# Kernel tuning notes

Measured on AMD Instinct MI355X. Metric: run time of the kernel, lower is better.

Reference implementation:

```python
import jax, jax.numpy as jnp
import numpy as np
import math

B, S, E, D = 8, 2048, 1024, 1024  # batch, seq, emb_dim, encoder_emb_dim
LN_EPS = 1e-5
CLAMP = 1.0e9

def setup_inputs() -> dict:
    key = jax.random.key(0)
    ks = jax.random.split(key, 6)
    s = 1.0 / math.sqrt(E)
    return {
        "x": jax.random.normal(ks[0], (B, S, E), dtype=jnp.float32),
        "ln_w": jnp.ones((E,), jnp.float32),
        "ln_b": jnp.zeros((E,), jnp.float32),
        "wq": jax.random.normal(ks[1], (E, D), jnp.float32) * s,
        "bq": jnp.zeros((D,), jnp.float32),
        "wk": jax.random.normal(ks[2], (E, D), jnp.float32) * s,
        "bk": jnp.zeros((D,), jnp.float32),
        "wv": jax.random.normal(ks[3], (E, D), jnp.float32) * s,
        "bv": jnp.zeros((D,), jnp.float32),
        "w0": jax.random.normal(ks[4], (D, E), jnp.float32) * (1.0 / math.sqrt(D)),
        "b0": jnp.zeros((E,), jnp.float32),
    }

def reference(x, ln_w, ln_b, wq, bq, wk, bk, wv, bv, w0, b0):
    # LayerNorm over last dim (torch default eps=1e-5)
    mu = jnp.mean(x, axis=-1, keepdims=True)
    var = jnp.mean(jnp.square(x - mu), axis=-1, keepdims=True)
    xn = (x - mu) * jax.lax.rsqrt(var + LN_EPS) * ln_w + ln_b

    q = xn @ wq + bq  # [B,S,D]
    k = xn @ wk + bk
    v = xn @ wv + bv

    scale = math.sqrt(D) + 1e-9
    scores = jnp.einsum("bsd,btd->bst", q, k) / scale
    scores = jnp.clip(scores, -CLAMP, CLAMP)

    # masking=True, self_attending=True: mask = tril(ones, diagonal=-1)
    # i.e. positions t < s get -inf; diagonal stays unmasked (no NaN rows).
    mask = jnp.tril(jnp.ones((S, S), dtype=bool), k=-1)
    scores = jnp.where(mask, -jnp.inf, scores)

    a = jax.nn.softmax(scores, axis=-1)
    h = jnp.einsum("bst,btd->bsd", a, v)
    return h @ w0 + b0
```

## Files before the change

### kernel.cpp

```cpp
#include <hip/hip_runtime.h>
#include <cmath>

using u16 = unsigned short;
using u32 = unsigned int;
using bf16x8 = __attribute__((ext_vector_type(8))) __bf16;
using f32x4  = __attribute__((ext_vector_type(4))) float;

__device__ inline u16 f2bf(float f) {
  u32 u = __float_as_uint(f);
  u32 r = (u + 0x7fffu + ((u >> 16) & 1u)) >> 16;
  return (u16)r;
}
__device__ inline float bf2f(u16 v) { return __uint_as_float(((u32)v) << 16); }

__global__ __launch_bounds__(256) void prep1(
    const float* __restrict__ x, const float* __restrict__ lnw,
    const float* __restrict__ lnb, const float* __restrict__ wq,
    const float* __restrict__ wk, const float* __restrict__ wv,
    const float* __restrict__ w0, const float* __restrict__ bq,
    const float* __restrict__ bk, const float* __restrict__ bv,
    u16* __restrict__ xn, u16* __restrict__ w0t, u16* __restrict__ wqb,
    u16* __restrict__ wkb, u16* __restrict__ wvb, float* __restrict__ uvec,
    float* __restrict__ vvec, float* __restrict__ wb, float* __restrict__ sb) {
  int b = blockIdx.x;
  int tid = threadIdx.x;
  __shared__ float red[4];
  __shared__ float red2[4];
  int lane = tid & 63, wave = tid >> 6;
  if (b < 16384) {
    const float4* xr = (const float4*)(x + (size_t)b * 1024);
    float4 v = xr[tid];
    float s  = v.x + v.y + v.z + v.w;
    float ss = v.x * v.x + v.y * v.y + v.z * v.z + v.w * v.w;
#pragma unroll
    for (int o = 32; o >= 1; o >>= 1) {
      s  += __shfl_xor(s, o, 64);
      ss += __shfl_xor(ss, o, 64);
    }
    if (lane == 0) { red[wave] = s; red2[wave] = ss; }
    __syncthreads();
    s  = red[0] + red[1] + red[2] + red[3];
    ss = red2[0] + red2[1] + red2[2] + red2[3];
    float mean = s * (1.0f / 1024.0f);
    float var  = ss * (1.0f / 1024.0f) - mean * mean;
    float rstd = rsqrtf(var + 1e-5f);
    int c = tid * 4;
    ushort4 ov;
    ov.x = f2bf((v.x - mean) * rstd * lnw[c + 0] + lnb[c + 0]);
    ov.y = f2bf((v.y - mean) * rstd * lnw[c + 1] + lnb[c + 1]);
    ov.z = f2bf((v.z - mean) * rstd * lnw[c + 2] + lnb[c + 2]);
    ov.w = f2bf((v.w - mean) * rstd * lnw[c + 3] + lnb[c + 3]);
    ((ushort4*)(xn + (size_t)b * 1024))[tid] = ov;
  } else if (b < 17408) {
    int b2 = b - 16384;
    int c0 = (b2 & 31) * 32, r0 = (b2 >> 5) * 32;
    int tx = tid & 31, ty = tid >> 5;
    __shared__ float tile[32][33];
#pragma unroll
    for (int i = 0; i < 32; i += 8)
      tile[ty + i][tx] = w0[(size_t)(r0 + ty + i) * 1024 + c0 + tx];
    __syncthreads();
#pragma unroll
    for (int i = 0; i < 32; i += 8)
      w0t[(size_t)(c0 + ty + i) * 1024 + r0 + tx] = f2bf(tile[tx][ty + i]);
  } else if (b < 18944) {
    int b3 = b - 17408;
    int mat = b3 / 512, blk = b3 % 512;
    const float* src = (mat == 0) ? wq : (mat == 1) ? wk : wv;
    u16* dst = (mat == 0) ? wqb : (mat == 1) ? wkb : wvb;
    size_t base = (size_t)blk * 2048 + (size_t)tid * 8;
#pragma unroll
    for (int i = 0; i < 8; ++i) dst[base + i] = f2bf(src[base + i]);
  } else if (b < 22016) {
    int b4 = b - 18944;
    int which = b4 >> 10, idx = b4 & 1023;
    float p = 0.f;
    if (which == 0) {
      const float* r = wq + (size_t)idx * 1024;
      for (int e = tid * 4; e < (tid + 1) * 4; ++e) p += r[e] * bk[e];
    } else if (which == 1) {
      const float* r = wk + (size_t)idx * 1024;
      for (int e = tid * 4; e < (tid + 1) * 4; ++e) p += r[e] * bq[e];
    } else {
      for (int d = tid * 4; d < (tid + 1) * 4; ++d)
        p += bv[d] * w0[(size_t)d * 1024 + idx];
    }
#pragma unroll
    for (int o = 32; o >= 1; o >>= 1) p += __shfl_xor(p, o, 64);
    if (lane == 0) red[wave] = p;
    __syncthreads();
    if (tid == 0) {
      float t = red[0] + red[1] + red[2] + red[3];
      if (which == 0) uvec[idx] = t;
      else if (which == 1) vvec[idx] = t;
      else wb[idx] = t;
    }
  } else {
    float p = 0.f;
    for (int e = tid * 4; e < (tid + 1) * 4; ++e) p += bq[e] * bk[e];
#pragma unroll
    for (int o = 32; o >= 1; o >>= 1) p += __shfl_xor(p, o, 64);
    if (lane == 0) red[wave] = p;
    __syncthreads();
    if (tid == 0) sb[0] = red[0] + red[1] + red[2] + red[3];
  }
}

__global__ __launch_bounds__(512) void ruv_kernel(
    const u16* __restrict__ xn, const float* __restrict__ uvec,
    const float* __restrict__ vvec, const float* __restrict__ sb,
    float* __restrict__ ru, float* __restrict__ rv) {
  int wv = threadIdx.x >> 6, lane = threadIdx.x & 63;
  int r = blockIdx.x * 8 + wv;
  const u16* row = xn + (size_t)r * 1024;
  int c0 = lane * 16;
  float pu = 0.f, pv = 0.f;
#pragma unroll
  for (int i = 0; i < 16; ++i) {
    float xv = bf2f(row[c0 + i]);
    pu += xv * uvec[c0 + i];
    pv += xv * vvec[c0 + i];
  }
#pragma unroll
  for (int o = 32; o >= 1; o >>= 1) {
    pu += __shfl_xor(pu, o, 64);
    pv += __shfl_xor(pv, o, 64);
  }
  if (lane == 0) { ru[r] = pu + sb[0]; rv[r] = pv; }
}

template <int OUTF32, int MODE>
__global__ __launch_bounds__(512, 2) void gemm256(
    const u16* __restrict__ A, const u16* __restrict__ B, void* __restrict__ Cv,
    const float* __restrict__ bias, int K, int lda, int ldb, int ldc,
    float scale, long long sA, long long sB, long long sC) {
  int gx = gridDim.x;
  int wg = blockIdx.y * gx + blockIdx.x;
  {
    int nwg = gx * gridDim.y;
    if ((nwg & 7) == 0) {
      int q = nwg >> 3;
      wg = (wg & 7) * q + (wg >> 3);
    }
  }
  const int ti = wg / gx, tj = wg % gx, bz = blockIdx.z;
  if (MODE == 1 && tj < ti) return;

  const u16* Ab = A + (size_t)bz * (size_t)sA;
  const u16* Bb = B + (size_t)bz * (size_t)sB;

  __shared__ u16 As[2][256 * 64];
  __shared__ u16 Bs[2][256 * 64];

  const int tid = threadIdx.x;
  const int wave = tid >> 6, lane = tid & 63;
  const int wr = wave >> 2, wc = wave & 3;
  const int fr = lane & 15;
  const int kb16 = (lane >> 4) * 16;
  const int swz = (fr & 7) << 4;
  const int cs0 = kb16 ^ swz;
  const int cs1 = (64 + kb16) ^ swz;
  const int aRowOff = (wr * 128 + fr) * 128;
  const int bRowOff = (wc * 64 + fr) * 128;

  size_t gAo[2][2], gBo[2][2];
  u32 ldsA[2][2], ldsB[2][2];
#pragma unroll
  for (int h = 0; h < 2; ++h) {
#pragma unroll
    for (int l = 0; l < 2; ++l) {
      int i = l * 512 + tid;
      int rih = i >> 3, ch8 = i & 7;
      int rA = (rih & 63) + ((rih >> 6) << 7) + h * 64;
      int cbA = (ch8 << 4) ^ ((rA & 7) << 4);
      gAo[h][l] = (size_t)rA * lda + (cbA >> 1);
      ldsA[h][l] = (u32)(rA * 8 + ch8) * 16;
      int rB = (rih & 31) + ((rih >> 5) << 6) + h * 32;
      int cbB = (ch8 << 4) ^ ((rB & 7) << 4);
      gBo[h][l] = (size_t)rB * ldb + (cbB >> 1);
      ldsB[h][l] = (u32)(rB * 8 + ch8) * 16;
    }
  }
  const size_t aBase = (size_t)(ti * 256) * lda;
  const size_t bBase = (size_t)(tj * 256) * ldb;

  const int k0 = (MODE == 2) ? ti * 256 : 0;
  const int niter = (K - k0) / 128;

  f32x4 acc[8][4] = {};
  bf16x8 aF[4][2], bF[4][2];

#define GLL(gaddr, laddr)                                        \
  __builtin_amdgcn_global_load_lds(                              \
      (const __attribute__((address_space(1))) void*)(gaddr),    \
      (__attribute__((address_space(3))) void*)(laddr), 16, 0, 0)

#define STAGE_A(buf, h, t)                                                     \
  do {                                                                         \
    const size_t _kt = aBase + (size_t)(k0 + (t) * 64);                        \
    GLL(Ab + _kt + gAo[h][0], (char*)&As[buf][0] + ldsA[h][0]);                \
    GLL(Ab + _kt + gAo[h][1], (char*)&As[buf][0] + ldsA[h][1]);                \
  } while (0)
#define STAGE_B(buf, h, t)                                                     \
  do {                                                                         \
    const size_t _kt = bBase + (size_t)(k0 + (t) * 64);                        \
    GLL(Bb + _kt + gBo[h][0], (char*)&Bs[buf][0] + ldsB[h][0]);                \
    GLL(Bb + _kt + gBo[h][1], (char*)&Bs[buf][0] + ldsB[h][1]);                \
  } while (0)

#define DS_A(buf, qm)                                                \
  do {                                                               \
    const char* _pa = (const char*)&As[buf][0] + aRowOff + (qm)*8192;\
    _Pragma("unroll") for (int mm = 0; mm < 4; ++mm) {               \
      aF[mm][0] = *(const bf16x8*)(_pa + mm * 2048 + cs0);           \
      aF[mm][1] = *(const bf16x8*)(_pa + mm * 2048 + cs1);           \
    }                                                                \
  } while (0)
#define DS_B(buf, nh)                                                \
  do {                                                               \
    const char* _pb = (const char*)&Bs[buf][0] + bRowOff;            \
    _Pragma("unroll") for (int nn = 0; nn < 2; ++nn) {               \
      bF[(nh)*2 + nn][0] = *(const bf16x8*)(_pb + ((nh)*2 + nn) * 2048 + cs0); \
      bF[(nh)*2 + nn][1] = *(const bf16x8*)(_pb + ((nh)*2 + nn) * 2048 + cs1); \
    }                                                                \
  } while (0)

#define MMA(qm, nh)                                                          \
  do {                                                                       \
    _Pragma("unroll") for (int mm = 0; mm < 4; ++mm)                         \
    _Pragma("unroll") for (int nn = 0; nn < 2; ++nn) {                       \
      f32x4 _c = acc[(qm)*4 + mm][(nh)*2 + nn];                              \
      _c = __builtin_amdgcn_mfma_f32_16x16x32_bf16(aF[mm][0], bF[(nh)*2+nn][0], _c, 0, 0, 0); \
      _c = __builtin_amdgcn_mfma_f32_16x16x32_bf16(aF[mm][1], bF[(nh)*2+nn][1], _c, 0, 0, 0); \
      acc[(qm)*4 + mm][(nh)*2 + nn] = _c;                                    \
    }                                                                        \
  } while (0)

#define BAR __builtin_amdgcn_s_barrier()
#define LGKM0 asm volatile("s_waitcnt lgkmcnt(0)" ::: "memory")
#define VM6 asm volatile("s_waitcnt vmcnt(6)" ::: "memory")
#define VM0 asm volatile("s_waitcnt vmcnt(0)" ::: "memory")
#define PRIO1 __builtin_amdgcn_s_setprio(1)
#define PRIO0 __builtin_amdgcn_s_setprio(0)

  STAGE_B(0, 0, 0); STAGE_B(0, 1, 0); STAGE_A(0, 0, 0); STAGE_A(0, 1, 0);
  STAGE_B(1, 0, 1); STAGE_B(1, 1, 1); STAGE_A(1, 0, 1);
  VM6; BAR;

  for (int it = 0; it < niter; ++it) {
    const bool last = (it == niter - 1);
    const int t1g = 2 * it + 1, t2g = 2 * it + 2, t3g = 2 * it + 3;

    DS_A(0, 0); DS_B(0, 0);
    STAGE_A(1, 1, t1g);
    BAR; LGKM0; PRIO1; MMA(0, 0); PRIO0; BAR;
    DS_B(0, 1);
    if (!last) STAGE_B(0, 0, t2g);
    BAR; LGKM0; PRIO1; MMA(0, 1); PRIO0; BAR;
    DS_A(0, 1);
    if (!last) STAGE_B(0, 1, t2g);
    BAR; LGKM0; PRIO1; MMA(1, 0); PRIO0; BAR;
    if (!last) STAGE_A(0, 0, t2g);
    BAR; PRIO1; MMA(1, 1); PRIO0;
    if (last) { VM0; } else { VM6; }
    BAR;
    DS_A(1, 0); DS_B(1, 0);
    if (!last) STAGE_A(0, 1, t2g);
    BAR; LGKM0; PRIO1; MMA(0, 0); PRIO0; BAR;
    DS_B(1, 1);
    if (!last) STAGE_B(1, 0, t3g);
    BAR; LGKM0; PRIO1; MMA(0, 1); PRIO0; BAR;
    DS_A(1, 1);
    if (!last) STAGE_B(1, 1, t3g);
    BAR; LGKM0; PRIO1; MMA(1, 0); PRIO0; BAR;
    if (!last) STAGE_A(1, 0, t3g);
    BAR; PRIO1; MMA(1, 1); PRIO0;
    if (!last) VM6;
    BAR;
  }

  const int orow0 = ti * 256 + wr * 128 + ((lane >> 4) << 2);
  const int ocol0 = tj * 256 + wc * 64 + fr;
#pragma unroll
  for (int m = 0; m < 8; ++m) {
#pragma unroll
    for (int n = 0; n < 4; ++n) {
      const int col = ocol0 + n * 16;
      const float bv = bias ? bias[col] : 0.0f;
#pragma unroll
      for (int j = 0; j < 4; ++j) {
        const int row = orow0 + m * 16 + j;
        const float v = acc[m][n][j] * scale + bv;
        const size_t idx = (size_t)bz * (size_t)sC + (size_t)row * ldc + col;
        if (OUTF32) ((float*)Cv)[idx] = v;
        else        ((u16*)Cv)[idx]   = f2bf(v);
      }
    }
  }
#undef GLL
#undef STAGE_A
#undef STAGE_B
#undef DS_A
#undef DS_B
#undef MMA
#undef BAR
#undef LGKM0
#undef VM6
#undef VM0
#undef PRIO1
#undef PRIO0
}

template <int BM, int EPI, int LDA, int LDB, int LDC, int KK, int K0CT>
__device__ __forceinline__ void gemm_body(
    const u16* __restrict__ Ab, const u16* __restrict__ Bb,
    void* __restrict__ Cp, const float* __restrict__ bias,
    const float* __restrict__ rbias, int rk0, float scale, size_t cbase,
    int ti, int tj, u16* __restrict__ AsP, u16* __restrict__ BsP,
    float* __restrict__ sumP, int dco,
    const float* __restrict__ ruP, const float* __restrict__ rvP) {
  constexpr int WM = BM / 2;
  constexpr int MH = BM / 64;
  constexpr int FM = 2 * MH;
  constexpr int HR = BM / 4;
  constexpr int LA = BM / 128;

  const int k0 = (K0CT >= 0) ? K0CT : rk0;

  const int tid = threadIdx.x;
  const int wave = tid >> 6, lane = tid & 63;
  const int wr = wave >> 2, wc = wave & 3;
  const int fr = lane & 15;
  const int kb16 = (lane >> 4) * 16;
  const int swz = (fr & 7) << 4;
  const int cs0 = kb16 ^ swz;
  const int cs1 = (64 + kb16) ^ swz;
  const int aRowOff = (wr * WM + fr) * 128;
  const int bRowOff = (wc * 64 + fr) * 128;

  __shared__ float invLds[(EPI == 2) ? BM : 1];
  if constexpr (EPI == 2) {
    if (tid < BM) {
      int s = ti * BM + tid;
      float a = 0.f;
      for (int q2 = s >> 8; q2 < 8; ++q2) a += sumP[q2 * 2048 + s];
      invLds[tid] = 1.0f / a;
    }
  }

  size_t gAo[2][LA], gBo[2][2];
  u32 ldsA[2][LA], ldsB[2][2];
#pragma unroll
  for (int h = 0; h < 2; ++h) {
#pragma unroll
    for (int l = 0; l < LA; ++l) {
      int i = l * 512 + tid;
      int rih = i >> 3, ch8 = i & 7;
      int rA = (rih % HR) + (rih / HR) * WM + h * HR;
      int cbA = (ch8 << 4) ^ ((rA & 7) << 4);
      gAo[h][l] = (size_t)rA * LDA + (cbA >> 1);
      ldsA[h][l] = (u32)(rA * 8 + ch8) * 16;
    }
#pragma unroll
    for (int l = 0; l < 2; ++l) {
      int i = l * 512 + tid;
      int rih = i >> 3, ch8 = i & 7;
      int rB = (rih & 31) + ((rih >> 5) << 6) + h * 32;
      int cbB = (ch8 << 4) ^ ((rB & 7) << 4);
      gBo[h][l] = (size_t)rB * LDB + (cbB >> 1);
      ldsB[h][l] = (u32)(rB * 8 + ch8) * 16;
    }
  }
  const size_t aBase = (size_t)(ti * BM) * LDA;
  const size_t bBase = (size_t)(tj * 256) * LDB;
  const int niter = (KK - k0) / 128;

  f32x4 acc[FM][4] = {};
  bf16x8 aF[MH][2], bF[4][2];

#define GLL(gaddr, laddr)                                        \
  __builtin_amdgcn_global_load_lds(                              \
      (const __attribute__((address_space(1))) void*)(gaddr),    \
      (__attribute__((address_space(3))) void*)(laddr), 16, 0, 0)

#define STAGE_A(buf, h, t)                                                   \
  do {                                                                       \
    const size_t _kt = aBase + (size_t)(k0 + (t) * 64);                      \
    _Pragma("unroll") for (int _l = 0; _l < LA; ++_l)                        \
        GLL(Ab + _kt + gAo[h][_l],                                           \
            (char*)(AsP + (buf) * (BM * 64)) + ldsA[h][_l]);                 \
  } while (0)
#define STAGE_B(buf, h, t)                                                   \
  do {                                                                       \
    const size_t _kt = bBase + (size_t)(k0 + (t) * 64);                      \
    _Pragma("unroll") for (int _l = 0; _l < 2; ++_l)                         \
        GLL(Bb + _kt + gBo[h][_l],                                           \
            (char*)(BsP + (buf) * (256 * 64)) + ldsB[h][_l]);                \
  } while (0)

#define DS_A(buf, qm)                                                        \
  do {                                                                       \
    const char* _pa =                                                        \
        (const char*)(AsP + (buf) * (BM * 64)) + aRowOff + (qm) * (MH * 2048); \
    _Pragma("unroll") for (int mm = 0; mm < MH; ++mm) {                      \
      aF[mm][0] = *(const bf16x8*)(_pa + mm * 2048 + cs0);                   \
      aF[mm][1] = *(const bf16x8*)(_pa + mm * 2048 + cs1);                   \
    }                                                                        \
  } while (0)
#define DS_B(buf, nh)                                                        \
  do {                                                                       \
    const char* _pb = (const char*)(BsP + (buf) * (256 * 64)) + bRowOff;     \
    _Pragma("unroll") for (int nn = 0; nn < 2; ++nn) {                       \
      bF[(nh)*2 + nn][0] = *(const bf16x8*)(_pb + ((nh)*2 + nn) * 2048 + cs0); \
      bF[(nh)*2 + nn][1] = *(const bf16x8*)(_pb + ((nh)*2 + nn) * 2048 + cs1); \
    }                                                                        \
  } while (0)

#define MMA(qm, nh)                                                          \
  do {                                                                       \
    _Pragma("unroll") for (int mm = 0; mm < MH; ++mm)                        \
    _Pragma("unroll") for (int nn = 0; nn < 2; ++nn) {                       \
      f32x4 _c = acc[(qm)*MH + mm][(nh)*2 + nn];                             \
      _c = __builtin_amdgcn_mfma_f32_16x16x32_bf16(aF[mm][0], bF[(nh)*2+nn][0], _c, 0, 0, 0); \
      _c = __builtin_amdgcn_mfma_f32_16x16x32_bf16(aF[mm][1], bF[(nh)*2+nn][1], _c, 0, 0, 0); \
      acc[(qm)*MH + mm][(nh)*2 + nn] = _c;                                   \
    }                                                                        \
  } while (0)

#define BAR __builtin_amdgcn_s_barrier()
#define LGKM0 asm volatile("s_waitcnt lgkmcnt(0)" ::: "memory")
#define VMN                                                                  \
  do {                                                                       \
    if constexpr (BM == 256)                                                 \
      asm volatile("s_waitcnt vmcnt(6)" ::: "memory");                       \
    else                                                                     \
      asm volatile("s_waitcnt vmcnt(5)" ::: "memory");                       \
  } while (0)
#define VM0 asm volatile("s_waitcnt vmcnt(0)" ::: "memory")
#define PRIO1 __builtin_amdgcn_s_setprio(1)
#define PRIO0 __builtin_amdgcn_s_setprio(0)

  STAGE_B(0, 0, 0); STAGE_B(0, 1, 0); STAGE_A(0, 0, 0); STAGE_A(0, 1, 0);
  STAGE_B(1, 0, 1); STAGE_B(1, 1, 1); STAGE_A(1, 0, 1);
  VMN; BAR;

#pragma unroll 1
  for (int it = 0; it < niter; ++it) {
    const bool last = (it == niter - 1);
    const int t1g = 2 * it + 1, t2g = 2 * it + 2, t3g = 2 * it + 3;

    DS_A(0, 0); DS_B(0, 0);
    STAGE_A(1, 1, t1g);
    BAR; LGKM0; PRIO1; MMA(0, 0); PRIO0; BAR;
    DS_B(0, 1);
    if (!last) STAGE_B(0, 0, t2g);
    BAR; LGKM0; PRIO1; MMA(0, 1); PRIO0; BAR;
    DS_A(0, 1);
    if (!last) STAGE_B(0, 1, t2g);
    BAR; LGKM0; PRIO1; MMA(1, 0); PRIO0; BAR;
    if (!last) STAGE_A(0, 0, t2g);
    BAR; PRIO1; MMA(1, 1); PRIO0;
    if (last) { VM0; } else { VMN; }
    BAR;
    DS_A(1, 0); DS_B(1, 0);
    if (!last) STAGE_A(0, 1, t2g);
    BAR; LGKM0; PRIO1; MMA(0, 0); PRIO0; BAR;
    DS_B(1, 1);
    if (!last) STAGE_B(1, 0, t3g);
    BAR; LGKM0; PRIO1; MMA(0, 1); PRIO0; BAR;
    DS_A(1, 1);
    if (!last) STAGE_B(1, 1, t3g);
    BAR; LGKM0; PRIO1; MMA(1, 0); PRIO0; BAR;
    if (!last) STAGE_A(1, 0, t3g);
    BAR; PRIO1; MMA(1, 1); PRIO0;
    if (!last) VMN;
    BAR;
  }

  const int orowL = wr * WM + ((lane >> 4) << 2);
  const int orow0 = ti * BM + orowL;
  const int ocol0 = tj * 256 + wc * 64 + fr;

  if constexpr (EPI == 1) {
    float* slds = (float*)AsP;
#pragma unroll
    for (int m = 0; m < FM; ++m) {
#pragma unroll
      for (int j = 0; j < 4; ++j) {
        const int rl = orowL + m * 16 + j;
        const int row = ti * BM + rl;
        const float ru = ruP[row];
        float rsum = 0.f;
#pragma unroll
        for (int n = 0; n < 4; ++n) {
          const int cl = wc * 64 + fr + n * 16;
          const int col = tj * 256 + cl;
          float v = (acc[m][n][j] + ru + rvP[col]) * scale;
          v = fminf(fmaxf(v, -1.0e9f), 1.0e9f);
          v = fminf(v, 60.0f);
          float e = __expf(v - 5.0f);
          if (cl < rl + dco) e = 0.f;
          rsum += e;
          ((u16*)Cp)[cbase + (size_t)row * LDC + col] = f2bf(e);
        }
        rsum += __shfl_xor(rsum, 1, 64);
        rsum += __shfl_xor(rsum, 2, 64);
        rsum += __shfl_xor(rsum, 4, 64);
        rsum += __shfl_xor(rsum, 8, 64);
        if (fr == 0) slds[rl * 4 + wc] = rsum;
      }
    }
    __syncthreads();
    if (tid < BM) {
      float t = slds[tid * 4 + 0] + slds[tid * 4 + 1] +
                slds[tid * 4 + 2] + slds[tid * 4 + 3];
      sumP[ti * BM + tid] = t;
    }
  } else {
#pragma unroll
    for (int m = 0; m < FM; ++m) {
#pragma unroll
      for (int j = 0; j < 4; ++j) {
        const int row = orow0 + m * 16 + j;
        float mul = (EPI == 2) ? invLds[orowL + m * 16 + j] : 1.0f;
        float rb = (EPI == 0 && rbias) ? rbias[row] : 0.0f;
#pragma unroll
        for (int n = 0; n < 4; ++n) {
          const int col = ocol0 + n * 16;
          const float bv = bias ? bias[col] : 0.0f;
          const size_t idx = cbase + (size_t)row * LDC + col;
          if constexpr (EPI == 2) {
            ((float*)Cp)[idx] = acc[m][n][j] * mul + bv;
          } else {
            ((u16*)Cp)[idx] = f2bf(acc[m][n][j] + bv + rb);
          }
        }
      }
    }
  }
#undef GLL
#undef STAGE_A
#undef STAGE_B
#undef DS_A
#undef DS_B
#undef MMA
#undef BAR
#undef LGKM0
#undef VMN
#undef VM0
#undef PRIO1
#undef PRIO0
}

__global__ __launch_bounds__(512, 2) void prep2(
    const u16* __restrict__ wqb, const u16* __restrict__ wkb,
    const u16* __restrict__ wvb, const u16* __restrict__ w0t,
    u16* __restrict__ Gt, u16* __restrict__ Uw) {
  __shared__ u16 As[2][128 * 64];
  __shared__ u16 Bs[2][256 * 64];
  int b = blockIdx.x;
  if (b < 32) {
    int ti = b & 7, tj = b >> 3;
    gemm_body<128, 0, 1024, 1024, 1024, 1024, 0>(
        wkb, wqb, Gt, nullptr, nullptr, 0, 1.0f, 0, ti, tj,
        &As[0][0], &Bs[0][0], nullptr, 0, nullptr, nullptr);
  } else {
    int b2 = b - 32;
    int ti = b2 & 7, tj = b2 >> 3;
    gemm_body<128, 0, 1024, 1024, 1024, 1024, 0>(
        w0t, wvb, Uw, nullptr, nullptr, 0, 1.0f, 0, ti, tj,
        &As[0][0], &Bs[0][0], nullptr, 0, nullptr, nullptr);
  }
}

__global__ __launch_bounds__(512, 2) void gemm_qkwt(
    const u16* __restrict__ xnG, const u16* __restrict__ xn,
    const u16* __restrict__ Uw, u16* __restrict__ Wt, u16* __restrict__ sc,
    float* __restrict__ sumP, const float* __restrict__ ru,
    const float* __restrict__ rv, const float* __restrict__ wb,
    int qkBlocks, int b0, int nb, float qk_scale) {
  __shared__ u16 As[2][256 * 64];
  __shared__ u16 Bs[2][256 * 64];
  const long long sXN = 2048LL * 1024, sWt = 1024LL * 2048, sS = 2048LL * 2048;
  int x = blockIdx.x;
  if (x < qkBlocks) {
    int bzl = x % nb, t36 = x / nb;
    int bz = b0 + bzl;
    int tq = 0, rem = t36;
    for (;;) { int L = 8 - tq; if (rem < L) break; rem -= L; ++tq; }
    int tj = tq + rem;
    gemm_body<256, 1, 1024, 1024, 2048, 1024, 0>(
        xnG + (size_t)bz * sXN, xn + (size_t)bz * sXN, sc, nullptr, nullptr,
        0, qk_scale, (size_t)bzl * sS, tq, tj, &As[0][0], &Bs[0][0],
        sumP + ((size_t)bz * 8 + tj) * 2048, (tq - tj) * 256,
        ru + (size_t)bz * 2048, rv + (size_t)bz * 2048);
  } else {
    int x2 = x - qkBlocks;
    int bz = x2 & 7;
    int o = x2 >> 3;
    int ti = o & 7, tj = o >> 3;
    gemm_body<128, 0, 1024, 1024, 2048, 1024, 0>(
        Uw, xn + (size_t)bz * sXN, Wt, nullptr, wb, 0, 1.0f,
        (size_t)bz * sWt, ti, tj, &As[0][0], &Bs[0][0],
        nullptr, 0, nullptr, nullptr);
  }
}

__global__ __launch_bounds__(512, 2) void gemm_pv(
    const u16* __restrict__ sc, const u16* __restrict__ Wt,
    float* __restrict__ out, const float* __restrict__ b0v,
    float* __restrict__ sumP, int nb, int bA) {
  __shared__ u16 As[2][128 * 64];
  __shared__ u16 Bs[2][256 * 64];
  int x = blockIdx.x;
  int bzl = x % nb;
  int rem = x / nb;
  int ti = rem >> 2, tj = rem & 3;
  int bz = bA + bzl;
  gemm_body<128, 2, 2048, 2048, 1024, 2048, -1>(
      sc + (size_t)bzl * 2048 * 2048, Wt + (size_t)bz * 1024 * 2048, out, b0v,
      nullptr, ti * 128, 1.0f, (size_t)bz * 2048 * 1024, ti, tj,
      &As[0][0], &Bs[0][0], sumP + (size_t)bz * 8 * 2048, 0,
      nullptr, nullptr);
}

extern "C" void kernel_launch(void* const* d_in, const int* in_sizes, int n_in,
                              void* d_out, int out_size, void* d_ws, size_t ws_size,
                              hipStream_t stream) {
  (void)in_sizes; (void)n_in; (void)out_size;
  const float* x   = (const float*)d_in[0];
  const float* lnw = (const float*)d_in[1];
  const float* lnb = (const float*)d_in[2];
  const float* wq  = (const float*)d_in[3];
  const float* bq  = (const float*)d_in[4];
  const float* wk  = (const float*)d_in[5];
  const float* bk  = (const float*)d_in[6];
  const float* wv  = (const float*)d_in[7];
  const float* bv  = (const float*)d_in[8];
  const float* w0  = (const float*)d_in[9];
  const float* b0  = (const float*)d_in[10];
  float* out = (float*)d_out;

  const size_t ROWS = 16384;
  char* ws = (char*)d_ws;
  size_t off = 0;
  auto alloc = [&](size_t bytes) -> void* {
    void* p = ws + off;
    off += (bytes + 255) & ~(size_t)255;
    return p;
  };
  u16*   xn   = (u16*)alloc(ROWS * 1024 * 2);
  u16*   w0t  = (u16*)alloc((size_t)1024 * 1024 * 2);
  u16*   wqb  = (u16*)alloc((size_t)1024 * 1024 * 2);
  u16*   wkb  = (u16*)alloc((size_t)1024 * 1024 * 2);
  u16*   wvb  = (u16*)alloc((size_t)1024 * 1024 * 2);
  u16*   Gt   = (u16*)alloc((size_t)1024 * 1024 * 2);
  u16*   Uw   = (u16*)alloc((size_t)1024 * 1024 * 2);
  float* uvec = (float*)alloc(1024 * 4);
  float* vvec = (float*)alloc(1024 * 4);
  float* wb   = (float*)alloc(1024 * 4);
  float* sb   = (float*)alloc(256);
  float* ru   = (float*)alloc(ROWS * 4);
  float* rv   = (float*)alloc(ROWS * 4);
  float* sumP = (float*)alloc((size_t)8 * 8 * 2048 * 4);
  u16*   xnG  = (u16*)alloc(ROWS * 1024 * 2);
  u16*   Wt   = (u16*)alloc(ROWS * 1024 * 2);

  const size_t CHUNK1 = (size_t)2048 * 2048 * 2;
  size_t avail = (ws_size > off) ? ws_size - off : 0;
  int NBCH = (int)(avail / CHUNK1);
  if (NBCH > 8) NBCH = 8;
  if (NBCH < 1) NBCH = 1;
  u16* sc = (u16*)(ws + off);

  prep1<<<dim3(22017), dim3(256), 0, stream>>>(
      x, lnw, lnb, wq, wk, wv, w0, bq, bk, bv,
      xn, w0t, wqb, wkb, wvb, uvec, vvec, wb, sb);
  prep2<<<dim3(64), dim3(512), 0, stream>>>(wqb, wkb, wvb, w0t, Gt, Uw);
  ruv_kernel<<<dim3(2048), dim3(512), 0, stream>>>(xn, uvec, vvec, sb, ru, rv);
  gemm256<0, 0><<<dim3(4, 64, 1), dim3(512), 0, stream>>>(
      xn, Gt, xnG, nullptr, 1024, 1024, 1024, 1024, 1.0f, 0, 0, 0);

  float qk_scale = (float)(1.0 / (std::sqrt(1024.0) + 1e-9));

  for (int bA = 0; bA < 8; bA += NBCH) {
    int nb = 8 - bA;
    if (nb > NBCH) nb = NBCH;
    int qkB = nb * 36;
    int wtB = (bA == 0) ? 512 : 0;
    gemm_qkwt<<<dim3(qkB + wtB), dim3(512), 0, stream>>>(
        xnG, xn, Uw, Wt, sc, sumP, ru, rv, wb, qkB, bA, nb, qk_scale);
    gemm_pv<<<dim3(64 * nb), dim3(512), 0, stream>>>(
        sc, Wt, out, b0, sumP, nb, bA);
  }
}
```

Before: 265.0 us.

## Use 256x256 tile kernel for PV GEMM and fold row-dot kernel into prep2

Replaces the 128-row PV GEMM with a dedicated 256x256-tile kernel. It skips the causally zero K range per row tile and applies the softmax normalization in its epilogue. The separate ruv row-dot kernel is merged into prep2 as extra blocks, which removes one launch. Larger tiles raise data reuse per block but give fewer blocks (32 per batch) and more register pressure. The PV blocks also carry uneven work because the K range each one covers varies.

```diff
diff --git a/kernel.cpp b/kernel.cpp
--- a/kernel.cpp
+++ b/kernel.cpp
@@ -104,29 +104,6 @@
     __syncthreads();
     if (tid == 0) sb[0] = red[0] + red[1] + red[2] + red[3];
   }
-}
-
-__global__ __launch_bounds__(512) void ruv_kernel(
-    const u16* __restrict__ xn, const float* __restrict__ uvec,
-    const float* __restrict__ vvec, const float* __restrict__ sb,
-    float* __restrict__ ru, float* __restrict__ rv) {
-  int wv = threadIdx.x >> 6, lane = threadIdx.x & 63;
-  int r = blockIdx.x * 8 + wv;
-  const u16* row = xn + (size_t)r * 1024;
-  int c0 = lane * 16;
-  float pu = 0.f, pv = 0.f;
-#pragma unroll
-  for (int i = 0; i < 16; ++i) {
-    float xv = bf2f(row[c0 + i]);
-    pu += xv * uvec[c0 + i];
-    pv += xv * vvec[c0 + i];
-  }
-#pragma unroll
-  for (int o = 32; o >= 1; o >>= 1) {
-    pu += __shfl_xor(pu, o, 64);
-    pv += __shfl_xor(pv, o, 64);
-  }
-  if (lane == 0) { ru[r] = pu + sb[0]; rv[r] = pv; }
 }
 
 template <int OUTF32, int MODE>
@@ -311,6 +288,199 @@
 #undef PRIO0
 }
 
+template <int OUTF32, int MODE>
+__global__ __launch_bounds__(512, 2) void gemm256_pv(
+    const u16* __restrict__ A, const u16* __restrict__ B, void* __restrict__ Cv,
+    const float* __restrict__ bias, int K, int lda, int ldb, int ldc,
+    float scale, long long sA, long long sB, long long sC,
+    const float* __restrict__ sumP) {
+  int gx = gridDim.x;
+  int wg = blockIdx.y * gx + blockIdx.x;
+  {
+    int nwg = gx * gridDim.y;
+    if ((nwg & 7) == 0) {
+      int q = nwg >> 3;
+      wg = (wg & 7) * q + (wg >> 3);
+    }
+  }
+  const int ti = wg / gx, tj = wg % gx, bz = blockIdx.z;
+  if (MODE == 1 && tj < ti) return;
+
+  const u16* Ab = A + (size_t)bz * (size_t)sA;
+  const u16* Bb = B + (size_t)bz * (size_t)sB;
+
+  __shared__ u16 As[2][256 * 64];
+  __shared__ u16 Bs[2][256 * 64];
+  __shared__ float invLds[256];
+
+  const int tid = threadIdx.x;
+  const int wave = tid >> 6, lane = tid & 63;
+  const int wr = wave >> 2, wc = wave & 3;
+  const int fr = lane & 15;
+  const int kb16 = (lane >> 4) * 16;
+  const int swz = (fr & 7) << 4;
+  const int cs0 = kb16 ^ swz;
+  const int cs1 = (64 + kb16) ^ swz;
+  const int aRowOff = (wr * 128 + fr) * 128;
+  const int bRowOff = (wc * 64 + fr) * 128;
+
+  size_t gAo[2][2], gBo[2][2];
+  u32 ldsA[2][2], ldsB[2][2];
+#pragma unroll
+  for (int h = 0; h < 2; ++h) {
+#pragma unroll
+    for (int l = 0; l < 2; ++l) {
+      int i = l * 512 + tid;
+      int rih = i >> 3, ch8 = i & 7;
+      int rA = (rih & 63) + ((rih >> 6) << 7) + h * 64;
+      int cbA = (ch8 << 4) ^ ((rA & 7) << 4);
+      gAo[h][l] = (size_t)rA * lda + (cbA >> 1);
+      ldsA[h][l] = (u32)(rA * 8 + ch8) * 16;
+      int rB = (rih & 31) + ((rih >> 5) << 6) + h * 32;
+      int cbB = (ch8 << 4) ^ ((rB & 7) << 4);
+      gBo[h][l] = (size_t)rB * ldb + (cbB >> 1);
+      ldsB[h][l] = (u32)(rB * 8 + ch8) * 16;
+    }
+  }
+  const size_t aBase = (size_t)(ti * 256) * lda;
+  const size_t bBase = (size_t)(tj * 256) * ldb;
+
+  const int k0 = (MODE == 2) ? ti * 256 : 0;
+  const int niter = (K - k0) / 128;
+
+  f32x4 acc[8][4] = {};
+  bf16x8 aF[4][2], bF[4][2];
+
+#define GLL(gaddr, laddr)                                        \
+  __builtin_amdgcn_global_load_lds(                              \
+      (const __attribute__((address_space(1))) void*)(gaddr),    \
+      (__attribute__((address_space(3))) void*)(laddr), 16, 0, 0)
+
+#define STAGE_A(buf, h, t)                                                     \
+  do {                                                                         \
+    const size_t _kt = aBase + (size_t)(k0 + (t) * 64);                        \
+    GLL(Ab + _kt + gAo[h][0], (char*)&As[buf][0] + ldsA[h][0]);                \
+    GLL(Ab + _kt + gAo[h][1], (char*)&As[buf][0] + ldsA[h][1]);                \
+  } while (0)
+#define STAGE_B(buf, h, t)                                                     \
+  do {                                                                         \
+    const size_t _kt = bBase + (size_t)(k0 + (t) * 64);                        \
+    GLL(Bb + _kt + gBo[h][0], (char*)&Bs[buf][0] + ldsB[h][0]);                \
+    GLL(Bb + _kt + gBo[h][1], (char*)&Bs[buf][0] + ldsB[h][1]);                \
+  } while (0)
+
+#define DS_A(buf, qm)                                                \
+  do {                                                               \
+    const char* _pa = (const char*)&As[buf][0] + aRowOff + (qm)*8192;\
+    _Pragma("unroll") for (int mm = 0; mm < 4; ++mm) {               \
+      aF[mm][0] = *(const bf16x8*)(_pa + mm * 2048 + cs0);           \
+      aF[mm][1] = *(const bf16x8*)(_pa + mm * 2048 + cs1);           \
+    }                                                                \
+  } while (0)
+#define DS_B(buf, nh)                                                \
+  do {                                                               \
+    const char* _pb = (const char*)&Bs[buf][0] + bRowOff;            \
+    _Pragma("unroll") for (int nn = 0; nn < 2; ++nn) {               \
+      bF[(nh)*2 + nn][0] = *(const bf16x8*)(_pb + ((nh)*2 + nn) * 2048 + cs0); \
+      bF[(nh)*2 + nn][1] = *(const bf16x8*)(_pb + ((nh)*2 + nn) * 2048 + cs1); \
+    }                                                                \
+  } while (0)
+
+#define MMA(qm, nh)                                                          \
+  do {                                                                       \
+    _Pragma("unroll") for (int mm = 0; mm < 4; ++mm)                         \
+    _Pragma("unroll") for (int nn = 0; nn < 2; ++nn) {                       \
+      f32x4 _c = acc[(qm)*4 + mm][(nh)*2 + nn];                              \
+      _c = __builtin_amdgcn_mfma_f32_16x16x32_bf16(aF[mm][0], bF[(nh)*2+nn][0], _c, 0, 0, 0); \
+      _c = __builtin_amdgcn_mfma_f32_16x16x32_bf16(aF[mm][1], bF[(nh)*2+nn][1], _c, 0, 0, 0); \
+      acc[(qm)*4 + mm][(nh)*2 + nn] = _c;                                    \
+    }                                                                        \
+  } while (0)
+
+#define BAR __builtin_amdgcn_s_barrier()
+#define LGKM0 asm volatile("s_waitcnt lgkmcnt(0)" ::: "memory")
+#define VM6 asm volatile("s_waitcnt vmcnt(6)" ::: "memory")
+#define VM0 asm volatile("s_waitcnt vmcnt(0)" ::: "memory")
+#define PRIO1 __builtin_amdgcn_s_setprio(1)
+#define PRIO0 __builtin_amdgcn_s_setprio(0)
+
+  STAGE_B(0, 0, 0); STAGE_B(0, 1, 0); STAGE_A(0, 0, 0); STAGE_A(0, 1, 0);
+  STAGE_B(1, 0, 1); STAGE_B(1, 1, 1); STAGE_A(1, 0, 1);
+  VM6; BAR;
+
+  for (int it = 0; it < niter; ++it) {
+    const bool last = (it == niter - 1);
+    const int t1g = 2 * it + 1, t2g = 2 * it + 2, t3g = 2 * it + 3;
+
+    DS_A(0, 0); DS_B(0, 0);
+    STAGE_A(1, 1, t1g);
+    BAR; LGKM0; PRIO1; MMA(0, 0); PRIO0; BAR;
+    DS_B(0, 1);
+    if (!last) STAGE_B(0, 0, t2g);
+    BAR; LGKM0; PRIO1; MMA(0, 1); PRIO0; BAR;
+    DS_A(0, 1);
+    if (!last) STAGE_B(0, 1, t2g);
+    BAR; LGKM0; PRIO1; MMA(1, 0); PRIO0; BAR;
+    if (!last) STAGE_A(0, 0, t2g);
+    BAR; PRIO1; MMA(1, 1); PRIO0;
+    if (last) { VM0; } else { VM6; }
+    BAR;
+    DS_A(1, 0); DS_B(1, 0);
+    if (!last) STAGE_A(0, 1, t2g);
+    BAR; LGKM0; PRIO1; MMA(0, 0); PRIO0; BAR;
+    DS_B(1, 1);
+    if (!last) STAGE_B(1, 0, t3g);
+    BAR; LGKM0; PRIO1; MMA(0, 1); PRIO0; BAR;
+    DS_A(1, 1);
+    if (!last) STAGE_B(1, 1, t3g);
+    BAR; LGKM0; PRIO1; MMA(1, 0); PRIO0; BAR;
+    if (!last) STAGE_A(1, 0, t3g);
+    BAR; PRIO1; MMA(1, 1); PRIO0;
+    if (!last) VM6;
+    BAR;
+  }
+
+  if (tid < 256) {
+    int s = ti * 256 + tid;
+    float a = 0.f;
+    for (int q2 = s >> 8; q2 < 8; ++q2)
+      a += sumP[(size_t)bz * 8 * 2048 + q2 * 2048 + s];
+    invLds[tid] = 1.0f / a;
+  }
+  __syncthreads();
+
+  const int orowL = wr * 128 + ((lane >> 4) << 2);
+  const int orow0 = ti * 256 + orowL;
+  const int ocol0 = tj * 256 + wc * 64 + fr;
+#pragma unroll
+  for (int m = 0; m < 8; ++m) {
+#pragma unroll
+    for (int n = 0; n < 4; ++n) {
+      const int col = ocol0 + n * 16;
+      const float bv = bias ? bias[col] : 0.0f;
+#pragma unroll
+      for (int j = 0; j < 4; ++j) {
+        const int row = orow0 + m * 16 + j;
+        const float v = acc[m][n][j] * invLds[orowL + m * 16 + j] + bv;
+        const size_t idx = (size_t)bz * (size_t)sC + (size_t)row * ldc + col;
+        ((float*)Cv)[idx] = v;
+      }
+    }
+  }
+#undef GLL
+#undef STAGE_A
+#undef STAGE_B
+#undef DS_A
+#undef DS_B
+#undef MMA
+#undef BAR
+#undef LGKM0
+#undef VM6
+#undef VM0
+#undef PRIO1
+#undef PRIO0
+}
+
 template <int BM, int EPI, int LDA, int LDB, int LDC, int KK, int K0CT>
 __device__ __forceinline__ void gemm_body(
     const u16* __restrict__ Ab, const u16* __restrict__ Bb,
@@ -337,16 +507,6 @@
   const int cs1 = (64 + kb16) ^ swz;
   const int aRowOff = (wr * WM + fr) * 128;
   const int bRowOff = (wc * 64 + fr) * 128;
-
-  __shared__ float invLds[(EPI == 2) ? BM : 1];
-  if constexpr (EPI == 2) {
-    if (tid < BM) {
-      int s = ti * BM + tid;
-      float a = 0.f;
-      for (int q2 = s >> 8; q2 < 8; ++q2) a += sumP[q2 * 2048 + s];
-      invLds[tid] = 1.0f / a;
-    }
-  }
 
   size_t gAo[2][LA], gBo[2][2];
   u32 ldsA[2][LA], ldsB[2][2];
@@ -522,18 +682,13 @@
 #pragma unroll
       for (int j = 0; j < 4; ++j) {
         const int row = orow0 + m * 16 + j;
-        float mul = (EPI == 2) ? invLds[orowL + m * 16 + j] : 1.0f;
-        float rb = (EPI == 0 && rbias) ? rbias[row] : 0.0f;
+        float rb = rbias ? rbias[row] : 0.0f;
 #pragma unroll
         for (int n = 0; n < 4; ++n) {
           const int col = ocol0 + n * 16;
           const float bv = bias ? bias[col] : 0.0f;
           const size_t idx = cbase + (size_t)row * LDC + col;
-          if constexpr (EPI == 2) {
-            ((float*)Cp)[idx] = acc[m][n][j] * mul + bv;
-          } else {
-            ((u16*)Cp)[idx] = f2bf(acc[m][n][j] + bv + rb);
-          }
+          ((u16*)Cp)[idx] = f2bf(acc[m][n][j] + bv + rb);
         }
       }
     }
@@ -555,7 +710,10 @@
 __global__ __launch_bounds__(512, 2) void prep2(
     const u16* __restrict__ wqb, const u16* __restrict__ wkb,
     const u16* __restrict__ wvb, const u16* __restrict__ w0t,
-    u16* __restrict__ Gt, u16* __restrict__ Uw) {
+    const u16* __restrict__ xn, const float* __restrict__ uvec,
+    const float* __restrict__ vvec, const float* __restrict__ sb,
+    u16* __restrict__ Gt, u16* __restrict__ Uw,
+    float* __restrict__ ru, float* __restrict__ rv) {
   __shared__ u16 As[2][128 * 64];
   __shared__ u16 Bs[2][256 * 64];
   int b = blockIdx.x;
@@ -564,12 +722,35 @@
     gemm_body<128, 0, 1024, 1024, 1024, 1024, 0>(
         wkb, wqb, Gt, nullptr, nullptr, 0, 1.0f, 0, ti, tj,
         &As[0][0], &Bs[0][0], nullptr, 0, nullptr, nullptr);
-  } else {
+  } else if (b < 64) {
     int b2 = b - 32;
     int ti = b2 & 7, tj = b2 >> 3;
     gemm_body<128, 0, 1024, 1024, 1024, 1024, 0>(
         w0t, wvb, Uw, nullptr, nullptr, 0, 1.0f, 0, ti, tj,
         &As[0][0], &Bs[0][0], nullptr, 0, nullptr, nullptr);
+  } else {
+    int b2 = b - 64;
+    int wv = threadIdx.x >> 6, lane = threadIdx.x & 63;
+    int rbase = b2 * 32 + wv * 4;
+#pragma unroll
+    for (int rr = 0; rr < 4; ++rr) {
+      int r = rbase + rr;
+      const u16* row = xn + (size_t)r * 1024;
+      int c0 = lane * 16;
+      float pu = 0.f, pv = 0.f;
+#pragma unroll
+      for (int i = 0; i < 16; ++i) {
+        float xv = bf2f(row[c0 + i]);
+        pu += xv * uvec[c0 + i];
+        pv += xv * vvec[c0 + i];
+      }
+#pragma unroll
+      for (int o = 32; o >= 1; o >>= 1) {
+        pu += __shfl_xor(pu, o, 64);
+        pv += __shfl_xor(pv, o, 64);
+      }
+      if (lane == 0) { ru[r] = pu + sb[0]; rv[r] = pv; }
+    }
   }
 }
 
@@ -606,24 +787,6 @@
   }
 }
 
-__global__ __launch_bounds__(512, 2) void gemm_pv(
-    const u16* __restrict__ sc, const u16* __restrict__ Wt,
-    float* __restrict__ out, const float* __restrict__ b0v,
-    float* __restrict__ sumP, int nb, int bA) {
-  __shared__ u16 As[2][128 * 64];
-  __shared__ u16 Bs[2][256 * 64];
-  int x = blockIdx.x;
-  int bzl = x % nb;
-  int rem = x / nb;
-  int ti = rem >> 2, tj = rem & 3;
-  int bz = bA + bzl;
-  gemm_body<128, 2, 2048, 2048, 1024, 2048, -1>(
-      sc + (size_t)bzl * 2048 * 2048, Wt + (size_t)bz * 1024 * 2048, out, b0v,
-      nullptr, ti * 128, 1.0f, (size_t)bz * 2048 * 1024, ti, tj,
-      &As[0][0], &Bs[0][0], sumP + (size_t)bz * 8 * 2048, 0,
-      nullptr, nullptr);
-}
-
 extern "C" void kernel_launch(void* const* d_in, const int* in_sizes, int n_in,
                               void* d_out, int out_size, void* d_ws, size_t ws_size,
                               hipStream_t stream) {
@@ -676,8 +839,8 @@
   prep1<<<dim3(22017), dim3(256), 0, stream>>>(
       x, lnw, lnb, wq, wk, wv, w0, bq, bk, bv,
       xn, w0t, wqb, wkb, wvb, uvec, vvec, wb, sb);
-  prep2<<<dim3(64), dim3(512), 0, stream>>>(wqb, wkb, wvb, w0t, Gt, Uw);
-  ruv_kernel<<<dim3(2048), dim3(512), 0, stream>>>(xn, uvec, vvec, sb, ru, rv);
+  prep2<<<dim3(576), dim3(512), 0, stream>>>(
+      wqb, wkb, wvb, w0t, xn, uvec, vvec, sb, Gt, Uw, ru, rv);
   gemm256<0, 0><<<dim3(4, 64, 1), dim3(512), 0, stream>>>(
       xn, Gt, xnG, nullptr, 1024, 1024, 1024, 1024, 1.0f, 0, 0, 0);
 
@@ -690,7 +853,10 @@
     int wtB = (bA == 0) ? 512 : 0;
     gemm_qkwt<<<dim3(qkB + wtB), dim3(512), 0, stream>>>(
         xnG, xn, Uw, Wt, sc, sumP, ru, rv, wb, qkB, bA, nb, qk_scale);
-    gemm_pv<<<dim3(64 * nb), dim3(512), 0, stream>>>(
-        sc, Wt, out, b0, sumP, nb, bA);
+    gemm256_pv<1, 2><<<dim3(4, 8, nb), dim3(512), 0, stream>>>(
+        sc, Wt + (size_t)bA * 1024 * 2048, (void*)(out + (size_t)bA * 2048 * 1024),
+        b0, 2048, 2048, 2048, 1024, 1.0f,
+        2048LL * 2048, 1024LL * 2048, 2048LL * 1024,
+        sumP + (size_t)bA * 8 * 2048);
   }
 }
```

Result: slower. 274.2 us (+3.5%).
